# Performance work log

Hardware: AMD Instinct MI355X
Metric: run time of the kernel (lower is better)

## Reference

```python
import jax, jax.numpy as jnp
import numpy as np

B, T, C = 4, 2048, 1024
H, HS = 16, 64  # n_heads, head_size; H*HS == C


def setup_inputs() -> dict:
    key = jax.random.key(0)
    ks = jax.random.split(key, 6)
    s = 0.02
    x = jax.random.normal(ks[0], (B, T, C), dtype=jnp.float32)
    Wq = jax.random.normal(ks[1], (H, C, HS), dtype=jnp.float32) * s
    Wk = jax.random.normal(ks[2], (H, C, HS), dtype=jnp.float32) * s
    Wv = jax.random.normal(ks[3], (H, C, HS), dtype=jnp.float32) * s
    Wo = jax.random.normal(ks[4], (C, C), dtype=jnp.float32) * s
    bo = jnp.zeros((C,), dtype=jnp.float32)
    return {"x": x, "Wq": Wq, "Wk": Wk, "Wv": Wv, "Wo": Wo, "bo": bo}


def reference(x, Wq, Wk, Wv, Wo, bo):
    # batched multi-head causal attention (math identical to per-head loop)
    q = jnp.einsum('btc,hcd->bhtd', x, Wq)  # [B,H,T,HS]
    k = jnp.einsum('btc,hcd->bhtd', x, Wk)
    v = jnp.einsum('btc,hcd->bhtd', x, Wv)
    scale = 1.0 / jnp.sqrt(jnp.asarray(HS, x.dtype))
    scores = jnp.einsum('bhtd,bhsd->bhts', q, k) * scale  # [B,H,T,T]
    causal = jnp.tril(jnp.ones((T, T), dtype=bool))
    scores = jnp.where(causal, scores, jnp.asarray(-jnp.inf, scores.dtype))
    attn = jax.nn.softmax(scores, axis=-1)
    out = jnp.einsum('bhts,bhsd->bhtd', attn, v)  # [B,H,T,HS]
    # concat heads along feature dim (head order == module list order)
    out = out.transpose(0, 2, 1, 3).reshape(B, T, C)
    return out @ Wo.T + bo
```

## Files before the change

### kernel.cpp

```cpp
#include <hip/hip_runtime.h>

typedef __attribute__((ext_vector_type(8))) short v8s;
typedef __attribute__((ext_vector_type(4))) short v4s;
typedef __attribute__((ext_vector_type(4))) float v4f;

static __device__ __forceinline__ short f2bf(float f) {
  union { float f; unsigned u; } c; c.f = f;
  unsigned r = c.u + 0x7fffu + ((c.u >> 16) & 1u);
  return (short)(r >> 16);
}

static __device__ __forceinline__ unsigned pk_bf16(float a, float b) {
  union { float f; unsigned u; } ca, cb; ca.f = a; cb.f = b;
  return ((ca.u + 0x8000u) >> 16) | ((cb.u + 0x8000u) & 0xffff0000u);
}

#if __has_builtin(__builtin_amdgcn_exp2f)
#define EXP2(x) __builtin_amdgcn_exp2f(x)
#else
#define EXP2(x) exp2f(x)
#endif

#define GLDS(gp, lp) __builtin_amdgcn_global_load_lds( \
    (const __attribute__((address_space(1))) void*)(gp), \
    (__attribute__((address_space(3))) void*)(lp), 16, 0, 0)


__global__ __launch_bounds__(256) void cast_f32_bf16(const float* __restrict__ src,
                                                     short* __restrict__ dst) {
  int idx = (blockIdx.x * 256 + threadIdx.x) * 4;
  float4 v = *(const float4*)(src + idx);
  v4s o; o.x = f2bf(v.x); o.y = f2bf(v.y); o.z = f2bf(v.z); o.w = f2bf(v.w);
  *(v4s*)(dst + idx) = o;
}

__global__ __launch_bounds__(256) void build_wt(const float* __restrict__ Wq,
                                                const float* __restrict__ Wk,
                                                const float* __restrict__ Wv,
                                                short* __restrict__ Wt) {
  __shared__ float tile[64][65];
  int blk = blockIdx.x;
  int sel = blk >> 8, rest = blk & 255;
  int h = rest >> 4, kt = rest & 15;
  const float* W = (sel == 0) ? Wq : ((sel == 1) ? Wk : Wv);
  int k0 = kt * 64;
  int tid = threadIdx.x;
  for (int i = 0; i < 4; ++i) {
    int c = i * 256 + tid;
    int row = c >> 4, c4 = (c & 15) * 4;
    float4 v = *(const float4*)(W + (size_t)h * 65536 + (size_t)(k0 + row) * 64 + c4);
    tile[row][c4 + 0] = v.x; tile[row][c4 + 1] = v.y;
    tile[row][c4 + 2] = v.z; tile[row][c4 + 3] = v.w;
  }
  __syncthreads();
  for (int i = 0; i < 2; ++i) {
    int c = i * 256 + tid;
    int d = c >> 3, k8 = (c & 7) * 8;
    v8s o;
    for (int j = 0; j < 8; ++j) o[j] = f2bf(tile[k8 + j][d]);
    *(v8s*)(Wt + (size_t)(sel * 1024 + h * 64 + d) * 1024 + k0 + k8) = o;
  }
}


__global__ __launch_bounds__(512) void gemm_qkv(const short* __restrict__ Xb,
                                                const short* __restrict__ Wt,
                                                short* __restrict__ Qo,
                                                short* __restrict__ Ko,
                                                short* __restrict__ Vt) {
  __shared__ short lds[49152];
  const int tid = threadIdx.x;
  const int lane = tid & 63, quad = lane >> 4, l16 = lane & 15;
  const int wave = tid >> 6;
  const int m0 = blockIdx.x * 256, n0 = blockIdx.y * 128;
  const int wm = (wave >> 1) * 64, wn = (wave & 1) * 64;

  const int r0 = tid >> 2, cbs = (tid & 3) ^ ((r0 >> 1) & 3);
  const size_t offA0 = (size_t)(m0 + r0) * 1024 + cbs * 8;
  const size_t offB0 = (size_t)(n0 + r0) * 1024 + cbs * 8;

  int aoff[4], boff[4];
#pragma unroll
  for (int mt = 0; mt < 4; ++mt) {
    int row = wm + mt * 16 + l16;
    aoff[mt] = row * 32 + (quad ^ ((row >> 1) & 3)) * 8;
  }
#pragma unroll
  for (int nt = 0; nt < 4; ++nt) {
    int row = wn + nt * 16 + l16;
    boff[nt] = row * 32 + (quad ^ ((row >> 1) & 3)) * 8;
  }

  v4f acc[4][4];
#pragma unroll
  for (int i = 0; i < 4; ++i)
#pragma unroll
    for (int j = 0; j < 4; ++j) acc[i][j] = (v4f){0.f, 0.f, 0.f, 0.f};

#pragma unroll
  for (int t = 0; t < 3; ++t) {
    GLDS(Xb + offA0 + t * 32, lds + t * 8192 + tid * 8);
    GLDS(Xb + offA0 + 131072 + t * 32, lds + t * 8192 + 4096 + tid * 8);
    GLDS(Wt + offB0 + t * 32, lds + 32768 + t * 4096 + tid * 8);
  }
  asm volatile("s_waitcnt vmcnt(6)" ::: "memory");
  __builtin_amdgcn_s_barrier();

#pragma unroll 4
  for (int t = 0; t < 32; ++t) {
    const int p = t & 3;
    int tn = t + 3; if (tn > 31) tn = 31;
    const int pn = (t + 3) & 3;
    const short* lAp = lds + p * 8192;
    const short* lBp = lds + 32768 + p * 4096;

    GLDS(Xb + offA0 + tn * 32, lds + pn * 8192 + tid * 8);
    GLDS(Xb + offA0 + 131072 + tn * 32, lds + pn * 8192 + 4096 + tid * 8);
    v8s a[4], b[2];
#pragma unroll
    for (int mt = 0; mt < 4; ++mt) a[mt] = *(const v8s*)(lAp + aoff[mt]);
    b[0] = *(const v8s*)(lBp + boff[0]);
    b[1] = *(const v8s*)(lBp + boff[1]);
    __builtin_amdgcn_s_setprio(1);
#pragma unroll
    for (int mt = 0; mt < 4; ++mt) {
      acc[mt][0] = __builtin_amdgcn_mfma_f32_16x16x32_bf16(a[mt], b[0], acc[mt][0], 0, 0, 0);
      acc[mt][1] = __builtin_amdgcn_mfma_f32_16x16x32_bf16(a[mt], b[1], acc[mt][1], 0, 0, 0);
    }
    __builtin_amdgcn_s_setprio(0);

    GLDS(Wt + offB0 + tn * 32, lds + 32768 + pn * 4096 + tid * 8);
    b[0] = *(const v8s*)(lBp + boff[2]);
    b[1] = *(const v8s*)(lBp + boff[3]);
    __builtin_amdgcn_s_setprio(1);
#pragma unroll
    for (int mt = 0; mt < 4; ++mt) {
      acc[mt][2] = __builtin_amdgcn_mfma_f32_16x16x32_bf16(a[mt], b[0], acc[mt][2], 0, 0, 0);
      acc[mt][3] = __builtin_amdgcn_mfma_f32_16x16x32_bf16(a[mt], b[1], acc[mt][3], 0, 0, 0);
    }
    __builtin_amdgcn_s_setprio(0);

    asm volatile("s_waitcnt vmcnt(6) lgkmcnt(0)" ::: "memory");
    __builtin_amdgcn_s_barrier();
  }

  const int selu = n0 >> 10;
  if (selu < 2) {
    short* obase = (selu == 0) ? Qo : Ko;
#pragma unroll
    for (int nt = 0; nt < 4; ++nt) {
      int n = (n0 + wn + nt * 16 + l16) & 1023;
      int h = n >> 6, d = n & 63;
#pragma unroll
      for (int mt = 0; mt < 4; ++mt) {
        int m = m0 + wm + mt * 16 + quad * 4;
        int b_ = m >> 11, tt = m & 2047;
        size_t base = (size_t)((b_ * 16 + h) * 2048 + tt) * 64 + d;
#pragma unroll
        for (int r = 0; r < 4; ++r)
          obase[base + (size_t)r * 64] = f2bf(acc[mt][nt][r]);
      }
    }
  } else {
#pragma unroll
    for (int nt = 0; nt < 4; ++nt) {
      int n = (n0 + wn + nt * 16 + l16) & 1023;
      int h = n >> 6, d = n & 63;
#pragma unroll
      for (int mt = 0; mt < 4; ++mt) {
        int m = m0 + wm + mt * 16 + quad * 4;
        int b_ = m >> 11, tt = m & 2047;
        int2 dw;
        dw.x = (int)pk_bf16(acc[mt][nt][0], acc[mt][nt][1]);
        dw.y = (int)pk_bf16(acc[mt][nt][2], acc[mt][nt][3]);
        *(int2*)(Vt + ((size_t)(b_ * 16 + h) * 64 + d) * 2048 + tt) = dw;
      }
    }
  }
}


__global__ __launch_bounds__(256, 2) void attn(const short* __restrict__ Q,
                                               const short* __restrict__ K,
                                               const short* __restrict__ Vt,
                                               short* __restrict__ AO) {
  __shared__ short lK[64 * 64];
  __shared__ short lV[64 * 64];
  __shared__ short lP[4 * 32 * 72];
  const int tid = threadIdx.x;
  const int w = tid >> 6, lane = tid & 63, quad = lane >> 4, l16 = lane & 15;
  const int bh = blockIdx.x & 63, pr = blockIdx.x >> 6;
  const float kexp = 0.18033688011112042f;
  const unsigned psel = 0x07060302u;
  short* pw = lP + w * (32 * 72);
  const size_t qkbase = (size_t)bh * 2048 * 64;
  const size_t vtbase = (size_t)bh * 64 * 2048;
  const int b_ = bh >> 4, h = bh & 15;

  const int r0 = tid >> 3, cp = tid & 7;
  const int cl0 = cp ^ (r0 & 7);
  const int r1 = r0 + 32;
  const int cl1 = cp ^ (r1 & 7);

  const int swz = l16 & 7;
  const int ph0 = (quad ^ swz) * 8;
  const int ph1 = ((quad + 4) ^ swz) * 8;

  for (int phase = 0; phase < 2; ++phase) {
    const int c = phase ? (15 - pr) : pr;
    const int qc = c * 128 + w * 32;

    v8s bQ[2][2];
#pragma unroll
    for (int qs = 0; qs < 2; ++qs) {
      const short* qb = Q + qkbase + (size_t)(qc + qs * 16 + l16) * 64 + quad * 8;
      bQ[qs][0] = *(const v8s*)(qb);
      bQ[qs][1] = *(const v8s*)(qb + 32);
    }
    v4f accO[2][4];
#pragma unroll
    for (int qs = 0; qs < 2; ++qs)
      for (int g = 0; g < 4; ++g) accO[qs][g] = (v4f){0.f, 0.f, 0.f, 0.f};
    float lrun[2] = {0.f, 0.f};

    const int nst = 2 * c + 2;
    for (int kt = 0; kt < nst; ++kt) {
      const int kb = kt * 64;
      __syncthreads();
      GLDS(K + qkbase + (size_t)(kb + r0) * 64 + cl0 * 8, lK + tid * 8);
      GLDS(K + qkbase + (size_t)(kb + r1) * 64 + cl1 * 8, lK + tid * 8 + 2048);
      GLDS(Vt + vtbase + (size_t)r0 * 2048 + kb + cl0 * 8, lV + tid * 8);
      GLDS(Vt + vtbase + (size_t)r1 * 2048 + kb + cl1 * 8, lV + tid * 8 + 2048);
      __syncthreads();

      const bool act0 = kb < qc + 16;
      const bool act1 = kb < qc + 32;
      if (!act1) continue;

      v8s aK[4][2];
#pragma unroll
      for (int mt = 0; mt < 4; ++mt) {
        const short* kr = lK + (mt * 16 + l16) * 64;
        aK[mt][0] = *(const v8s*)(kr + ph0);
        aK[mt][1] = *(const v8s*)(kr + ph1);
      }
#pragma unroll
      for (int qs = 0; qs < 2; ++qs) {
        if (qs == 0 ? !act0 : false) continue;
        const int rbase = qc + qs * 16;
        v4f sT[4];
#pragma unroll
        for (int mt = 0; mt < 4; ++mt) {
          v4f t = (v4f){0.f, 0.f, 0.f, 0.f};
          t = __builtin_amdgcn_mfma_f32_16x16x32_bf16(aK[mt][0], bQ[qs][0], t, 0, 0, 0);
          t = __builtin_amdgcn_mfma_f32_16x16x32_bf16(aK[mt][1], bQ[qs][1], t, 0, 0, 0);
          sT[mt] = t;
        }
        if (kb + 63 >= rbase) {
          const int kq = kb + quad * 4 - (rbase + l16);
#pragma unroll
          for (int mt = 0; mt < 4; ++mt)
#pragma unroll
            for (int r = 0; r < 4; ++r)
              if (kq + mt * 16 + r > 0) sT[mt][r] = -__builtin_inff();
        }
        float ls = lrun[qs];
#pragma unroll
        for (int mt = 0; mt < 4; ++mt) {
          float p0 = EXP2(sT[mt][0] * kexp);
          float p1 = EXP2(sT[mt][1] * kexp);
          float p2 = EXP2(sT[mt][2] * kexp);
          float p3 = EXP2(sT[mt][3] * kexp);
          ls += (p0 + p1) + (p2 + p3);
          int2 dw;
          dw.x = (int)__builtin_amdgcn_perm(__float_as_uint(p1), __float_as_uint(p0), psel);
          dw.y = (int)__builtin_amdgcn_perm(__float_as_uint(p3), __float_as_uint(p2), psel);
          *(int2*)&pw[(qs * 16 + l16) * 72 + mt * 16 + quad * 4] = dw;
        }
        lrun[qs] = ls;
      }
      v8s aV[4][2];
#pragma unroll
      for (int g = 0; g < 4; ++g) {
        const short* vr = lV + (g * 16 + l16) * 64;
        aV[g][0] = *(const v8s*)(vr + ph0);
        aV[g][1] = *(const v8s*)(vr + ph1);
      }
#pragma unroll
      for (int qs = 0; qs < 2; ++qs) {
        if (qs == 0 ? !act0 : false) continue;
        v8s bP0 = *(const v8s*)&pw[(qs * 16 + l16) * 72 + quad * 8];
        v8s bP1 = *(const v8s*)&pw[(qs * 16 + l16) * 72 + 32 + quad * 8];
#pragma unroll
        for (int g = 0; g < 4; ++g) {
          accO[qs][g] = __builtin_amdgcn_mfma_f32_16x16x32_bf16(aV[g][0], bP0, accO[qs][g], 0, 0, 0);
          accO[qs][g] = __builtin_amdgcn_mfma_f32_16x16x32_bf16(aV[g][1], bP1, accO[qs][g], 0, 0, 0);
        }
      }
    }

#pragma unroll
    for (int qs = 0; qs < 2; ++qs) {
      float ls = lrun[qs];
      ls += __shfl_xor(ls, 16);
      ls += __shfl_xor(ls, 32);
      float inv = __builtin_amdgcn_rcpf(ls);
      int t = qc + qs * 16 + l16;
      short* ao = AO + ((size_t)(b_ * 2048 + t)) * 1024 + h * 64 + quad * 4;
#pragma unroll
      for (int g = 0; g < 4; ++g) {
        int2 dw;
        dw.x = (int)pk_bf16(accO[qs][g][0] * inv, accO[qs][g][1] * inv);
        dw.y = (int)pk_bf16(accO[qs][g][2] * inv, accO[qs][g][3] * inv);
        *(int2*)(ao + g * 16) = dw;
      }
    }
  }
}


__global__ __launch_bounds__(256) void gemm_out(const short* __restrict__ AO,
                                                const short* __restrict__ Wot,
                                                const float* __restrict__ bo,
                                                float* __restrict__ out) {
  __shared__ short lA[128 * 32];
  __shared__ short lB[128 * 32];
  const int tid = threadIdx.x;
  const int lane = tid & 63, quad = lane >> 4, l16 = lane & 15;
  const int wave = tid >> 6;
  const int m0 = blockIdx.x * 128, n0 = blockIdx.y * 128;
  const int wm = (wave >> 1) * 64, wn = (wave & 1) * 64;
  v4f acc[4][4];
  for (int i = 0; i < 4; ++i)
    for (int j = 0; j < 4; ++j) acc[i][j] = (v4f){0.f, 0.f, 0.f, 0.f};

  for (int k0 = 0; k0 < 1024; k0 += 32) {
    __syncthreads();
    for (int i = 0; i < 2; ++i) {
      int c = i * 256 + tid;
      int row = c >> 2, kc = c & 3;
      GLDS(AO + (size_t)(m0 + row) * 1024 + k0 + kc * 8, lA + c * 8);
      GLDS(Wot + (size_t)(n0 + row) * 1024 + k0 + kc * 8, lB + c * 8);
    }
    __syncthreads();
    v8s a[4], b[4];
    for (int mt = 0; mt < 4; ++mt) a[mt] = *(const v8s*)&lA[(wm + mt * 16 + l16) * 32 + quad * 8];
    for (int nt = 0; nt < 4; ++nt) b[nt] = *(const v8s*)&lB[(wn + nt * 16 + l16) * 32 + quad * 8];
    for (int mt = 0; mt < 4; ++mt)
      for (int nt = 0; nt < 4; ++nt)
        acc[mt][nt] = __builtin_amdgcn_mfma_f32_16x16x32_bf16(a[mt], b[nt], acc[mt][nt], 0, 0, 0);
  }

  for (int nt = 0; nt < 4; ++nt) {
    int n = n0 + wn + nt * 16 + l16;
    float bias = bo[n];
    for (int mt = 0; mt < 4; ++mt)
      for (int r = 0; r < 4; ++r) {
        int m = m0 + wm + mt * 16 + quad * 4 + r;
        out[(size_t)m * 1024 + n] = acc[mt][nt][r] + bias;
      }
  }
}


extern "C" void kernel_launch(void* const* d_in, const int* in_sizes, int n_in,
                              void* d_out, int out_size, void* d_ws, size_t ws_size,
                              hipStream_t stream) {
  const float* x  = (const float*)d_in[0];
  const float* Wq = (const float*)d_in[1];
  const float* Wk = (const float*)d_in[2];
  const float* Wv = (const float*)d_in[3];
  const float* Wo = (const float*)d_in[4];
  const float* bo = (const float*)d_in[5];
  float* out = (float*)d_out;
  char* ws = (char*)d_ws;

  short* Xb  = (short*)(ws);
  short* Wt  = (short*)(ws + (16u << 20));
  short* Wot = (short*)(ws + (22u << 20));
  short* Q   = (short*)(ws + (24u << 20));
  short* K   = (short*)(ws + (40u << 20));
  short* Vt  = (short*)(ws + (56u << 20));

  cast_f32_bf16<<<8192, 256, 0, stream>>>(x, Xb);
  cast_f32_bf16<<<1024, 256, 0, stream>>>(Wo, Wot);
  build_wt<<<768, 256, 0, stream>>>(Wq, Wk, Wv, Wt);
  gemm_qkv<<<dim3(32, 24), 512, 0, stream>>>(Xb, Wt, Q, K, Vt);
  attn<<<dim3(512), 256, 0, stream>>>(Q, K, Vt, Xb);
  gemm_out<<<dim3(64, 8), 256, 0, stream>>>(Xb, Wot, bo, out);
}
```

Baseline: 243.0 us.

## Restructure QKV GEMM pipeline with XCD-aware tiling and enlarge attention query tiles

The QKV GEMM moves to a K-step of 64, a double-buffered LDS schedule with interleaved barriers and set-priority phases, and a block-index remap that groups tiles per XCD for L2 locality. The attention kernel drops the two-phase paired-chunk loop: each block now handles one 256-row query chunk, with each wave covering 64 rows, and chunks are mapped so blocks with complementary causal work are paired. The aim is fewer global K/V reloads per query row and more MFMA work per barrier. The cost is higher register pressure (accO grows to 4x4) and possible load imbalance across blocks.

```diff
diff --git a/kernel.cpp b/kernel.cpp
--- a/kernel.cpp
+++ b/kernel.cpp
@@ -63,6 +63,55 @@
 }
 
 
+#define GQ_STAGE_A(P, T) do {                                                     \
+  _Pragma("unroll") for (int i_ = 0; i_ < 4; ++i_)                                \
+    GLDS(Xb + (size_t)(m0 + rA + i_ * 64) * 1024 + (T) * 64 + cbl * 8,            \
+         lds + (P) * 16384 + (tid + i_ * 512) * 8); } while (0)
+
+#define GQ_STAGE_B(P, T) do {                                                     \
+  _Pragma("unroll") for (int i_ = 0; i_ < 2; ++i_)                                \
+    GLDS(Wt + (size_t)(n0 + rA + i_ * 64) * 1024 + (T) * 64 + cbl * 8,            \
+         lds + 32768 + (P) * 8192 + (tid + i_ * 512) * 8); } while (0)
+
+#define PH_MID()                                                                  \
+  __builtin_amdgcn_s_barrier();                                                   \
+  asm volatile("s_waitcnt lgkmcnt(0)" ::: "memory");                              \
+  __builtin_amdgcn_sched_barrier(0);                                              \
+  __builtin_amdgcn_s_setprio(1)
+
+#define PH_END()                                                                  \
+  __builtin_amdgcn_s_setprio(0);                                                  \
+  __builtin_amdgcn_s_barrier()
+
+#define LD_A(P, KS) _Pragma("unroll") for (int mt = 0; mt < 4; ++mt)              \
+    a[mt] = *(const v8s*)(lds + (P) * 16384 + arow[mt] + ((KS) ? csw1 : csw0));
+
+#define LD_B2(P, N0, KS)                                                          \
+  bb[0] = *(const v8s*)(lds + 32768 + (P) * 8192 + brow[N0] + ((KS) ? csw1 : csw0)); \
+  bb[1] = *(const v8s*)(lds + 32768 + (P) * 8192 + brow[(N0) + 1] + ((KS) ? csw1 : csw0));
+
+#define MF2(N0) _Pragma("unroll") for (int mt = 0; mt < 4; ++mt) {                \
+    acc[mt][N0] = __builtin_amdgcn_mfma_f32_16x16x32_bf16(a[mt], bb[0], acc[mt][N0], 0, 0, 0); \
+    acc[mt][(N0) + 1] = __builtin_amdgcn_mfma_f32_16x16x32_bf16(a[mt], bb[1], acc[mt][(N0) + 1], 0, 0, 0); }
+
+#define KTILE(P, T) {                                                             \
+  const int q_ = (P) ^ 1;                                                         \
+  const int tn1 = ((T) + 1 < 16) ? (T) + 1 : 15;                                  \
+  const int tn2 = ((T) + 2 < 16) ? (T) + 2 : 15;                                  \
+  LD_A(P, 0); LD_B2(P, 0, 0);                                                     \
+  GQ_STAGE_B(q_, tn1);                                                            \
+  PH_MID(); MF2(0); PH_END();                                                     \
+  LD_B2(P, 2, 0);                                                                 \
+  PH_MID(); MF2(2); PH_END();                                                     \
+  LD_A(P, 1); LD_B2(P, 0, 1);                                                     \
+  PH_MID(); MF2(0); PH_END();                                                     \
+  LD_B2(P, 2, 1);                                                                 \
+  GQ_STAGE_A(P, tn2);                                                             \
+  PH_MID(); MF2(2);                                                               \
+  __builtin_amdgcn_s_setprio(0);                                                  \
+  asm volatile("s_waitcnt vmcnt(4)" ::: "memory");                                \
+  __builtin_amdgcn_s_barrier(); }
+
 __global__ __launch_bounds__(512) void gemm_qkv(const short* __restrict__ Xb,
                                                 const short* __restrict__ Wt,
                                                 short* __restrict__ Qo,
@@ -72,77 +121,42 @@
   const int tid = threadIdx.x;
   const int lane = tid & 63, quad = lane >> 4, l16 = lane & 15;
   const int wave = tid >> 6;
-  const int m0 = blockIdx.x * 256, n0 = blockIdx.y * 128;
+  const int bid = blockIdx.x;
+  const int xcd = bid & 7, rr = bid >> 3;
+  const int m0 = ((xcd >> 1) * 8 + (rr & 7)) * 256;
+  const int n0 = ((xcd & 1) * 12 + (rr >> 3)) * 128;
   const int wm = (wave >> 1) * 64, wn = (wave & 1) * 64;
 
-  const int r0 = tid >> 2, cbs = (tid & 3) ^ ((r0 >> 1) & 3);
-  const size_t offA0 = (size_t)(m0 + r0) * 1024 + cbs * 8;
-  const size_t offB0 = (size_t)(n0 + r0) * 1024 + cbs * 8;
-
-  int aoff[4], boff[4];
-#pragma unroll
-  for (int mt = 0; mt < 4; ++mt) {
-    int row = wm + mt * 16 + l16;
-    aoff[mt] = row * 32 + (quad ^ ((row >> 1) & 3)) * 8;
-  }
-#pragma unroll
-  for (int nt = 0; nt < 4; ++nt) {
-    int row = wn + nt * 16 + l16;
-    boff[nt] = row * 32 + (quad ^ ((row >> 1) & 3)) * 8;
-  }
+  const int rA = tid >> 3;
+  const int cbl = (tid & 7) ^ (rA & 7);
+
+  const int swz = l16 & 7;
+  const int csw0 = (quad ^ swz) * 8;
+  const int csw1 = ((4 + quad) ^ swz) * 8;
+  int arow[4], brow[4];
+#pragma unroll
+  for (int mt = 0; mt < 4; ++mt) arow[mt] = (wm + mt * 16 + l16) * 64;
+#pragma unroll
+  for (int nt = 0; nt < 4; ++nt) brow[nt] = (wn + nt * 16 + l16) * 64;
 
   v4f acc[4][4];
 #pragma unroll
   for (int i = 0; i < 4; ++i)
 #pragma unroll
     for (int j = 0; j < 4; ++j) acc[i][j] = (v4f){0.f, 0.f, 0.f, 0.f};
-
-#pragma unroll
-  for (int t = 0; t < 3; ++t) {
-    GLDS(Xb + offA0 + t * 32, lds + t * 8192 + tid * 8);
-    GLDS(Xb + offA0 + 131072 + t * 32, lds + t * 8192 + 4096 + tid * 8);
-    GLDS(Wt + offB0 + t * 32, lds + 32768 + t * 4096 + tid * 8);
-  }
-  asm volatile("s_waitcnt vmcnt(6)" ::: "memory");
+  v8s a[4], bb[2];
+
+  GQ_STAGE_A(0, 0); GQ_STAGE_B(0, 0); GQ_STAGE_A(1, 1);
+  asm volatile("s_waitcnt vmcnt(4)" ::: "memory");
   __builtin_amdgcn_s_barrier();
 
-#pragma unroll 4
-  for (int t = 0; t < 32; ++t) {
-    const int p = t & 3;
-    int tn = t + 3; if (tn > 31) tn = 31;
-    const int pn = (t + 3) & 3;
-    const short* lAp = lds + p * 8192;
-    const short* lBp = lds + 32768 + p * 4096;
-
-    GLDS(Xb + offA0 + tn * 32, lds + pn * 8192 + tid * 8);
-    GLDS(Xb + offA0 + 131072 + tn * 32, lds + pn * 8192 + 4096 + tid * 8);
-    v8s a[4], b[2];
-#pragma unroll
-    for (int mt = 0; mt < 4; ++mt) a[mt] = *(const v8s*)(lAp + aoff[mt]);
-    b[0] = *(const v8s*)(lBp + boff[0]);
-    b[1] = *(const v8s*)(lBp + boff[1]);
-    __builtin_amdgcn_s_setprio(1);
-#pragma unroll
-    for (int mt = 0; mt < 4; ++mt) {
-      acc[mt][0] = __builtin_amdgcn_mfma_f32_16x16x32_bf16(a[mt], b[0], acc[mt][0], 0, 0, 0);
-      acc[mt][1] = __builtin_amdgcn_mfma_f32_16x16x32_bf16(a[mt], b[1], acc[mt][1], 0, 0, 0);
-    }
-    __builtin_amdgcn_s_setprio(0);
-
-    GLDS(Wt + offB0 + tn * 32, lds + 32768 + pn * 4096 + tid * 8);
-    b[0] = *(const v8s*)(lBp + boff[2]);
-    b[1] = *(const v8s*)(lBp + boff[3]);
-    __builtin_amdgcn_s_setprio(1);
-#pragma unroll
-    for (int mt = 0; mt < 4; ++mt) {
-      acc[mt][2] = __builtin_amdgcn_mfma_f32_16x16x32_bf16(a[mt], b[0], acc[mt][2], 0, 0, 0);
-      acc[mt][3] = __builtin_amdgcn_mfma_f32_16x16x32_bf16(a[mt], b[1], acc[mt][3], 0, 0, 0);
-    }
-    __builtin_amdgcn_s_setprio(0);
-
-    asm volatile("s_waitcnt vmcnt(6) lgkmcnt(0)" ::: "memory");
-    __builtin_amdgcn_s_barrier();
-  }
+#pragma unroll 1
+  for (int tt = 0; tt < 8; ++tt) {
+    const int t0 = tt * 2;
+    KTILE(0, t0);
+    KTILE(1, t0 + 1);
+  }
+  asm volatile("s_waitcnt vmcnt(0)" ::: "memory");
 
   const int selu = n0 >> 10;
   if (selu < 2) {
@@ -154,8 +168,8 @@
 #pragma unroll
       for (int mt = 0; mt < 4; ++mt) {
         int m = m0 + wm + mt * 16 + quad * 4;
-        int b_ = m >> 11, tt = m & 2047;
-        size_t base = (size_t)((b_ * 16 + h) * 2048 + tt) * 64 + d;
+        int b_ = m >> 11, tt_ = m & 2047;
+        size_t base = (size_t)((b_ * 16 + h) * 2048 + tt_) * 64 + d;
 #pragma unroll
         for (int r = 0; r < 4; ++r)
           obase[base + (size_t)r * 64] = f2bf(acc[mt][nt][r]);
@@ -169,15 +183,24 @@
 #pragma unroll
       for (int mt = 0; mt < 4; ++mt) {
         int m = m0 + wm + mt * 16 + quad * 4;
-        int b_ = m >> 11, tt = m & 2047;
+        int b_ = m >> 11, tt_ = m & 2047;
         int2 dw;
         dw.x = (int)pk_bf16(acc[mt][nt][0], acc[mt][nt][1]);
         dw.y = (int)pk_bf16(acc[mt][nt][2], acc[mt][nt][3]);
-        *(int2*)(Vt + ((size_t)(b_ * 16 + h) * 64 + d) * 2048 + tt) = dw;
-      }
-    }
-  }
-}
+        *(int2*)(Vt + ((size_t)(b_ * 16 + h) * 64 + d) * 2048 + tt_) = dw;
+      }
+    }
+  }
+}
+
+#undef KTILE
+#undef LD_A
+#undef LD_B2
+#undef MF2
+#undef PH_MID
+#undef PH_END
+#undef GQ_STAGE_A
+#undef GQ_STAGE_B
 
 
 __global__ __launch_bounds__(256, 2) void attn(const short* __restrict__ Q,
@@ -186,13 +209,15 @@
                                                short* __restrict__ AO) {
   __shared__ short lK[64 * 64];
   __shared__ short lV[64 * 64];
-  __shared__ short lP[4 * 32 * 72];
+  __shared__ short lP[4 * 64 * 72];
   const int tid = threadIdx.x;
   const int w = tid >> 6, lane = tid & 63, quad = lane >> 4, l16 = lane & 15;
-  const int bh = blockIdx.x & 63, pr = blockIdx.x >> 6;
+  const int bh = blockIdx.x & 63;
+  const int u = blockIdx.x >> 6;
+  const int c = (u < 4) ? u : 11 - u;
   const float kexp = 0.18033688011112042f;
   const unsigned psel = 0x07060302u;
-  short* pw = lP + w * (32 * 72);
+  short* pw = lP + w * (64 * 72);
   const size_t qkbase = (size_t)bh * 2048 * 64;
   const size_t vtbase = (size_t)bh * 64 * 2048;
   const int b_ = bh >> 4, h = bh & 15;
@@ -206,114 +231,114 @@
   const int ph0 = (quad ^ swz) * 8;
   const int ph1 = ((quad + 4) ^ swz) * 8;
 
-  for (int phase = 0; phase < 2; ++phase) {
-    const int c = phase ? (15 - pr) : pr;
-    const int qc = c * 128 + w * 32;
-
-    v8s bQ[2][2];
-#pragma unroll
-    for (int qs = 0; qs < 2; ++qs) {
-      const short* qb = Q + qkbase + (size_t)(qc + qs * 16 + l16) * 64 + quad * 8;
-      bQ[qs][0] = *(const v8s*)(qb);
-      bQ[qs][1] = *(const v8s*)(qb + 32);
-    }
-    v4f accO[2][4];
-#pragma unroll
-    for (int qs = 0; qs < 2; ++qs)
-      for (int g = 0; g < 4; ++g) accO[qs][g] = (v4f){0.f, 0.f, 0.f, 0.f};
-    float lrun[2] = {0.f, 0.f};
-
-    const int nst = 2 * c + 2;
-    for (int kt = 0; kt < nst; ++kt) {
-      const int kb = kt * 64;
-      __syncthreads();
-      GLDS(K + qkbase + (size_t)(kb + r0) * 64 + cl0 * 8, lK + tid * 8);
-      GLDS(K + qkbase + (size_t)(kb + r1) * 64 + cl1 * 8, lK + tid * 8 + 2048);
-      GLDS(Vt + vtbase + (size_t)r0 * 2048 + kb + cl0 * 8, lV + tid * 8);
-      GLDS(Vt + vtbase + (size_t)r1 * 2048 + kb + cl1 * 8, lV + tid * 8 + 2048);
-      __syncthreads();
-
-      const bool act0 = kb < qc + 16;
-      const bool act1 = kb < qc + 32;
-      if (!act1) continue;
-
-      v8s aK[4][2];
+  const int qc = c * 256 + w * 64;
+
+  v8s bQ[4][2];
+#pragma unroll
+  for (int qs = 0; qs < 4; ++qs) {
+    const short* qb = Q + qkbase + (size_t)(qc + qs * 16 + l16) * 64 + quad * 8;
+    bQ[qs][0] = *(const v8s*)(qb);
+    bQ[qs][1] = *(const v8s*)(qb + 32);
+  }
+  v4f accO[4][4];
+#pragma unroll
+  for (int qs = 0; qs < 4; ++qs)
+#pragma unroll
+    for (int g = 0; g < 4; ++g) accO[qs][g] = (v4f){0.f, 0.f, 0.f, 0.f};
+  float lrun[4] = {0.f, 0.f, 0.f, 0.f};
+
+  const int nst = 4 * c + 4;
+  for (int kt = 0; kt < nst; ++kt) {
+    const int kb = kt * 64;
+    __syncthreads();
+    GLDS(K + qkbase + (size_t)(kb + r0) * 64 + cl0 * 8, lK + tid * 8);
+    GLDS(K + qkbase + (size_t)(kb + r1) * 64 + cl1 * 8, lK + tid * 8 + 2048);
+    GLDS(Vt + vtbase + (size_t)r0 * 2048 + kb + cl0 * 8, lV + tid * 8);
+    GLDS(Vt + vtbase + (size_t)r1 * 2048 + kb + cl1 * 8, lV + tid * 8 + 2048);
+    __syncthreads();
+
+    if (kb >= qc + 64) continue;
+
+    v8s aK[4][2];
+#pragma unroll
+    for (int mt = 0; mt < 4; ++mt) {
+      const short* kr = lK + (mt * 16 + l16) * 64;
+      aK[mt][0] = *(const v8s*)(kr + ph0);
+      aK[mt][1] = *(const v8s*)(kr + ph1);
+    }
+#pragma unroll
+    for (int qs = 0; qs < 4; ++qs) {
+      const int rbase = qc + qs * 16;
+      if (kb >= rbase + 16) continue;
+      v4f sT[4];
+      __builtin_amdgcn_s_setprio(1);
 #pragma unroll
       for (int mt = 0; mt < 4; ++mt) {
-        const short* kr = lK + (mt * 16 + l16) * 64;
-        aK[mt][0] = *(const v8s*)(kr + ph0);
-        aK[mt][1] = *(const v8s*)(kr + ph1);
-      }
-#pragma unroll
-      for (int qs = 0; qs < 2; ++qs) {
-        if (qs == 0 ? !act0 : false) continue;
-        const int rbase = qc + qs * 16;
-        v4f sT[4];
-#pragma unroll
-        for (int mt = 0; mt < 4; ++mt) {
-          v4f t = (v4f){0.f, 0.f, 0.f, 0.f};
-          t = __builtin_amdgcn_mfma_f32_16x16x32_bf16(aK[mt][0], bQ[qs][0], t, 0, 0, 0);
-          t = __builtin_amdgcn_mfma_f32_16x16x32_bf16(aK[mt][1], bQ[qs][1], t, 0, 0, 0);
-          sT[mt] = t;
-        }
-        if (kb + 63 >= rbase) {
-          const int kq = kb + quad * 4 - (rbase + l16);
-#pragma unroll
-          for (int mt = 0; mt < 4; ++mt)
-#pragma unroll
-            for (int r = 0; r < 4; ++r)
-              if (kq + mt * 16 + r > 0) sT[mt][r] = -__builtin_inff();
-        }
-        float ls = lrun[qs];
-#pragma unroll
-        for (int mt = 0; mt < 4; ++mt) {
-          float p0 = EXP2(sT[mt][0] * kexp);
-          float p1 = EXP2(sT[mt][1] * kexp);
-          float p2 = EXP2(sT[mt][2] * kexp);
-          float p3 = EXP2(sT[mt][3] * kexp);
-          ls += (p0 + p1) + (p2 + p3);
-          int2 dw;
-          dw.x = (int)__builtin_amdgcn_perm(__float_as_uint(p1), __float_as_uint(p0), psel);
-          dw.y = (int)__builtin_amdgcn_perm(__float_as_uint(p3), __float_as_uint(p2), psel);
-          *(int2*)&pw[(qs * 16 + l16) * 72 + mt * 16 + quad * 4] = dw;
-        }
-        lrun[qs] = ls;
-      }
-      v8s aV[4][2];
+        v4f t = (v4f){0.f, 0.f, 0.f, 0.f};
+        t = __builtin_amdgcn_mfma_f32_16x16x32_bf16(aK[mt][0], bQ[qs][0], t, 0, 0, 0);
+        t = __builtin_amdgcn_mfma_f32_16x16x32_bf16(aK[mt][1], bQ[qs][1], t, 0, 0, 0);
+        sT[mt] = t;
+      }
+      __builtin_amdgcn_s_setprio(0);
+      if (kb + 63 >= rbase) {
+        const int kq = kb + quad * 4 - (rbase + l16);
+#pragma unroll
+        for (int mt = 0; mt < 4; ++mt)
+#pragma unroll
+          for (int r = 0; r < 4; ++r)
+            if (kq + mt * 16 + r > 0) sT[mt][r] = -__builtin_inff();
+      }
+      float ls = lrun[qs];
+#pragma unroll
+      for (int mt = 0; mt < 4; ++mt) {
+        float p0 = EXP2(sT[mt][0] * kexp);
+        float p1 = EXP2(sT[mt][1] * kexp);
+        float p2 = EXP2(sT[mt][2] * kexp);
+        float p3 = EXP2(sT[mt][3] * kexp);
+        ls += (p0 + p1) + (p2 + p3);
+        int2 dw;
+        dw.x = (int)__builtin_amdgcn_perm(__float_as_uint(p1), __float_as_uint(p0), psel);
+        dw.y = (int)__builtin_amdgcn_perm(__float_as_uint(p3), __float_as_uint(p2), psel);
+        *(int2*)&pw[(qs * 16 + l16) * 72 + mt * 16 + quad * 4] = dw;
+      }
+      lrun[qs] = ls;
+    }
+    v8s aV[4][2];
+#pragma unroll
+    for (int g = 0; g < 4; ++g) {
+      const short* vr = lV + (g * 16 + l16) * 64;
+      aV[g][0] = *(const v8s*)(vr + ph0);
+      aV[g][1] = *(const v8s*)(vr + ph1);
+    }
+#pragma unroll
+    for (int qs = 0; qs < 4; ++qs) {
+      if (kb >= qc + qs * 16 + 16) continue;
+      v8s bP0 = *(const v8s*)&pw[(qs * 16 + l16) * 72 + quad * 8];
+      v8s bP1 = *(const v8s*)&pw[(qs * 16 + l16) * 72 + 32 + quad * 8];
+      __builtin_amdgcn_s_setprio(1);
 #pragma unroll
       for (int g = 0; g < 4; ++g) {
-        const short* vr = lV + (g * 16 + l16) * 64;
-        aV[g][0] = *(const v8s*)(vr + ph0);
-        aV[g][1] = *(const v8s*)(vr + ph1);
-      }
-#pragma unroll
-      for (int qs = 0; qs < 2; ++qs) {
-        if (qs == 0 ? !act0 : false) continue;
-        v8s bP0 = *(const v8s*)&pw[(qs * 16 + l16) * 72 + quad * 8];
-        v8s bP1 = *(const v8s*)&pw[(qs * 16 + l16) * 72 + 32 + quad * 8];
-#pragma unroll
-        for (int g = 0; g < 4; ++g) {
-          accO[qs][g] = __builtin_amdgcn_mfma_f32_16x16x32_bf16(aV[g][0], bP0, accO[qs][g], 0, 0, 0);
-          accO[qs][g] = __builtin_amdgcn_mfma_f32_16x16x32_bf16(aV[g][1], bP1, accO[qs][g], 0, 0, 0);
-        }
-      }
-    }
-
-#pragma unroll
-    for (int qs = 0; qs < 2; ++qs) {
-      float ls = lrun[qs];
-      ls += __shfl_xor(ls, 16);
-      ls += __shfl_xor(ls, 32);
-      float inv = __builtin_amdgcn_rcpf(ls);
-      int t = qc + qs * 16 + l16;
-      short* ao = AO + ((size_t)(b_ * 2048 + t)) * 1024 + h * 64 + quad * 4;
-#pragma unroll
-      for (int g = 0; g < 4; ++g) {
-        int2 dw;
-        dw.x = (int)pk_bf16(accO[qs][g][0] * inv, accO[qs][g][1] * inv);
-        dw.y = (int)pk_bf16(accO[qs][g][2] * inv, accO[qs][g][3] * inv);
-        *(int2*)(ao + g * 16) = dw;
-      }
+        accO[qs][g] = __builtin_amdgcn_mfma_f32_16x16x32_bf16(aV[g][0], bP0, accO[qs][g], 0, 0, 0);
+        accO[qs][g] = __builtin_amdgcn_mfma_f32_16x16x32_bf16(aV[g][1], bP1, accO[qs][g], 0, 0, 0);
+      }
+      __builtin_amdgcn_s_setprio(0);
+    }
+  }
+
+#pragma unroll
+  for (int qs = 0; qs < 4; ++qs) {
+    float ls = lrun[qs];
+    ls += __shfl_xor(ls, 16);
+    ls += __shfl_xor(ls, 32);
+    float inv = __builtin_amdgcn_rcpf(ls);
+    int t = qc + qs * 16 + l16;
+    short* ao = AO + ((size_t)(b_ * 2048 + t)) * 1024 + h * 64 + quad * 4;
+#pragma unroll
+    for (int g = 0; g < 4; ++g) {
+      int2 dw;
+      dw.x = (int)pk_bf16(accO[qs][g][0] * inv, accO[qs][g][1] * inv);
+      dw.y = (int)pk_bf16(accO[qs][g][2] * inv, accO[qs][g][3] * inv);
+      *(int2*)(ao + g * 16) = dw;
     }
   }
 }
@@ -385,7 +410,7 @@
   cast_f32_bf16<<<8192, 256, 0, stream>>>(x, Xb);
   cast_f32_bf16<<<1024, 256, 0, stream>>>(Wo, Wot);
   build_wt<<<768, 256, 0, stream>>>(Wq, Wk, Wv, Wt);
-  gemm_qkv<<<dim3(32, 24), 512, 0, stream>>>(Xb, Wt, Q, K, Vt);
+  gemm_qkv<<<768, 512, 0, stream>>>(Xb, Wt, Q, K, Vt);
   attn<<<dim3(512), 256, 0, stream>>>(Q, K, Vt, Xb);
   gemm_out<<<dim3(64, 8), 256, 0, stream>>>(Xb, Wot, bo, out);
 }
```

Result: slower. 262.3 us (+7.9%).

## Fuse prep kernels, double-buffer attention K/V loads, pipeline output GEMM

Applied to the files above, without the earlier changes.

Three separate changes. The three preprocessing launches (x cast, Wo cast, QKV weight transpose) become a single prep kernel, which removes launch overhead. The attention kernel now double-buffers K/V tiles in LDS, prefetching the next tile before computing the current one, and raises wave priority around the MFMA blocks. The output GEMM moves to 512 threads, 256x128 tiles, a 4-stage LDS prefetch pipeline and swizzled LDS addressing. The extra LDS use in attention may reduce occupancy, and the partial waitcnt logic has to be exact to stay correct.

```diff
diff --git a/kernel.cpp b/kernel.cpp
--- a/kernel.cpp
+++ b/kernel.cpp
@@ -26,25 +26,32 @@
     (__attribute__((address_space(3))) void*)(lp), 16, 0, 0)
 
 
-__global__ __launch_bounds__(256) void cast_f32_bf16(const float* __restrict__ src,
-                                                     short* __restrict__ dst) {
-  int idx = (blockIdx.x * 256 + threadIdx.x) * 4;
-  float4 v = *(const float4*)(src + idx);
-  v4s o; o.x = f2bf(v.x); o.y = f2bf(v.y); o.z = f2bf(v.z); o.w = f2bf(v.w);
-  *(v4s*)(dst + idx) = o;
-}
-
-__global__ __launch_bounds__(256) void build_wt(const float* __restrict__ Wq,
-                                                const float* __restrict__ Wk,
-                                                const float* __restrict__ Wv,
-                                                short* __restrict__ Wt) {
+__global__ __launch_bounds__(256) void prep(const float* __restrict__ x,
+                                            const float* __restrict__ Wq,
+                                            const float* __restrict__ Wk,
+                                            const float* __restrict__ Wv,
+                                            const float* __restrict__ Wo,
+                                            short* __restrict__ Xb,
+                                            short* __restrict__ Wot,
+                                            short* __restrict__ Wt) {
   __shared__ float tile[64][65];
-  int blk = blockIdx.x;
-  int sel = blk >> 8, rest = blk & 255;
-  int h = rest >> 4, kt = rest & 15;
+  const int blk = blockIdx.x;
+  const int tid = threadIdx.x;
+  if (blk < 9216) {
+    const float* src = (blk < 8192) ? x : Wo;
+    short* dst = (blk < 8192) ? Xb : Wot;
+    const int b2 = (blk < 8192) ? blk : (blk - 8192);
+    const int idx = (b2 * 256 + tid) * 4;
+    float4 v = *(const float4*)(src + idx);
+    v4s o; o.x = f2bf(v.x); o.y = f2bf(v.y); o.z = f2bf(v.z); o.w = f2bf(v.w);
+    *(v4s*)(dst + idx) = o;
+    return;
+  }
+  const int bb = blk - 9216;
+  const int sel = bb >> 8, rest = bb & 255;
+  const int h = rest >> 4, kt = rest & 15;
   const float* W = (sel == 0) ? Wq : ((sel == 1) ? Wk : Wv);
-  int k0 = kt * 64;
-  int tid = threadIdx.x;
+  const int k0 = kt * 64;
   for (int i = 0; i < 4; ++i) {
     int c = i * 256 + tid;
     int row = c >> 4, c4 = (c & 15) * 4;
@@ -154,8 +161,8 @@
 #pragma unroll
       for (int mt = 0; mt < 4; ++mt) {
         int m = m0 + wm + mt * 16 + quad * 4;
-        int b_ = m >> 11, tt = m & 2047;
-        size_t base = (size_t)((b_ * 16 + h) * 2048 + tt) * 64 + d;
+        int b_ = m >> 11, tt_ = m & 2047;
+        size_t base = (size_t)((b_ * 16 + h) * 2048 + tt_) * 64 + d;
 #pragma unroll
         for (int r = 0; r < 4; ++r)
           obase[base + (size_t)r * 64] = f2bf(acc[mt][nt][r]);
@@ -169,23 +176,29 @@
 #pragma unroll
       for (int mt = 0; mt < 4; ++mt) {
         int m = m0 + wm + mt * 16 + quad * 4;
-        int b_ = m >> 11, tt = m & 2047;
+        int b_ = m >> 11, tt_ = m & 2047;
         int2 dw;
         dw.x = (int)pk_bf16(acc[mt][nt][0], acc[mt][nt][1]);
         dw.y = (int)pk_bf16(acc[mt][nt][2], acc[mt][nt][3]);
-        *(int2*)(Vt + ((size_t)(b_ * 16 + h) * 64 + d) * 2048 + tt) = dw;
+        *(int2*)(Vt + ((size_t)(b_ * 16 + h) * 64 + d) * 2048 + tt_) = dw;
       }
     }
   }
 }
 
+
+#define ASTAGE(P, KB)                                                             \
+  GLDS(K + qkbase + (size_t)((KB) + r0) * 64 + cl0 * 8, lK + (P) * 4096 + tid * 8);          \
+  GLDS(K + qkbase + (size_t)((KB) + r1) * 64 + cl1 * 8, lK + (P) * 4096 + tid * 8 + 2048);   \
+  GLDS(Vt + vtbase + (size_t)r0 * 2048 + (KB) + cl0 * 8, lV + (P) * 4096 + tid * 8);         \
+  GLDS(Vt + vtbase + (size_t)r1 * 2048 + (KB) + cl1 * 8, lV + (P) * 4096 + tid * 8 + 2048)
 
 __global__ __launch_bounds__(256, 2) void attn(const short* __restrict__ Q,
                                                const short* __restrict__ K,
                                                const short* __restrict__ Vt,
                                                short* __restrict__ AO) {
-  __shared__ short lK[64 * 64];
-  __shared__ short lV[64 * 64];
+  __shared__ short lK[2 * 64 * 64];
+  __shared__ short lV[2 * 64 * 64];
   __shared__ short lP[4 * 32 * 72];
   const int tid = threadIdx.x;
   const int w = tid >> 6, lane = tid & 63, quad = lane >> 4, l16 = lane & 15;
@@ -224,79 +237,92 @@
     float lrun[2] = {0.f, 0.f};
 
     const int nst = 2 * c + 2;
+
+    __builtin_amdgcn_s_barrier();
+    ASTAGE(0, 0);
+
     for (int kt = 0; kt < nst; ++kt) {
+      const int p = kt & 1;
       const int kb = kt * 64;
-      __syncthreads();
-      GLDS(K + qkbase + (size_t)(kb + r0) * 64 + cl0 * 8, lK + tid * 8);
-      GLDS(K + qkbase + (size_t)(kb + r1) * 64 + cl1 * 8, lK + tid * 8 + 2048);
-      GLDS(Vt + vtbase + (size_t)r0 * 2048 + kb + cl0 * 8, lV + tid * 8);
-      GLDS(Vt + vtbase + (size_t)r1 * 2048 + kb + cl1 * 8, lV + tid * 8 + 2048);
-      __syncthreads();
+      if (kt + 1 < nst) {
+        ASTAGE(p ^ 1, kb + 64);
+        asm volatile("s_waitcnt vmcnt(4)" ::: "memory");
+      } else {
+        asm volatile("s_waitcnt vmcnt(0)" ::: "memory");
+      }
+      __builtin_amdgcn_s_barrier();
+      const short* lKp = lK + p * 4096;
+      const short* lVp = lV + p * 4096;
 
       const bool act0 = kb < qc + 16;
       const bool act1 = kb < qc + 32;
-      if (!act1) continue;
-
-      v8s aK[4][2];
-#pragma unroll
-      for (int mt = 0; mt < 4; ++mt) {
-        const short* kr = lK + (mt * 16 + l16) * 64;
-        aK[mt][0] = *(const v8s*)(kr + ph0);
-        aK[mt][1] = *(const v8s*)(kr + ph1);
-      }
-#pragma unroll
-      for (int qs = 0; qs < 2; ++qs) {
-        if (qs == 0 ? !act0 : false) continue;
-        const int rbase = qc + qs * 16;
-        v4f sT[4];
+      if (act1) {
+        v8s aK[4][2];
 #pragma unroll
         for (int mt = 0; mt < 4; ++mt) {
-          v4f t = (v4f){0.f, 0.f, 0.f, 0.f};
-          t = __builtin_amdgcn_mfma_f32_16x16x32_bf16(aK[mt][0], bQ[qs][0], t, 0, 0, 0);
-          t = __builtin_amdgcn_mfma_f32_16x16x32_bf16(aK[mt][1], bQ[qs][1], t, 0, 0, 0);
-          sT[mt] = t;
+          const short* kr = lKp + (mt * 16 + l16) * 64;
+          aK[mt][0] = *(const v8s*)(kr + ph0);
+          aK[mt][1] = *(const v8s*)(kr + ph1);
         }
-        if (kb + 63 >= rbase) {
-          const int kq = kb + quad * 4 - (rbase + l16);
-#pragma unroll
-          for (int mt = 0; mt < 4; ++mt)
-#pragma unroll
-            for (int r = 0; r < 4; ++r)
-              if (kq + mt * 16 + r > 0) sT[mt][r] = -__builtin_inff();
+#pragma unroll
+        for (int qs = 0; qs < 2; ++qs) {
+          if (qs == 0 ? !act0 : false) continue;
+          const int rbase = qc + qs * 16;
+          v4f sT[4];
+          __builtin_amdgcn_s_setprio(1);
+#pragma unroll
+          for (int mt = 0; mt < 4; ++mt) {
+            v4f t = (v4f){0.f, 0.f, 0.f, 0.f};
+            t = __builtin_amdgcn_mfma_f32_16x16x32_bf16(aK[mt][0], bQ[qs][0], t, 0, 0, 0);
+            t = __builtin_amdgcn_mfma_f32_16x16x32_bf16(aK[mt][1], bQ[qs][1], t, 0, 0, 0);
+            sT[mt] = t;
+          }
+          __builtin_amdgcn_s_setprio(0);
+          if (kb + 63 >= rbase) {
+            const int kq = kb + quad * 4 - (rbase + l16);
+#pragma unroll
+            for (int mt = 0; mt < 4; ++mt)
+#pragma unroll
+              for (int r = 0; r < 4; ++r)
+                if (kq + mt * 16 + r > 0) sT[mt][r] = -__builtin_inff();
+          }
+          float ls = lrun[qs];
+#pragma unroll
+          for (int mt = 0; mt < 4; ++mt) {
+            float p0 = EXP2(sT[mt][0] * kexp);
+            float p1 = EXP2(sT[mt][1] * kexp);
+            float p2 = EXP2(sT[mt][2] * kexp);
+            float p3 = EXP2(sT[mt][3] * kexp);
+            ls += (p0 + p1) + (p2 + p3);
+            int2 dw;
+            dw.x = (int)__builtin_amdgcn_perm(__float_as_uint(p1), __float_as_uint(p0), psel);
+            dw.y = (int)__builtin_amdgcn_perm(__float_as_uint(p3), __float_as_uint(p2), psel);
+            *(int2*)&pw[(qs * 16 + l16) * 72 + mt * 16 + quad * 4] = dw;
+          }
+          lrun[qs] = ls;
         }
-        float ls = lrun[qs];
-#pragma unroll
-        for (int mt = 0; mt < 4; ++mt) {
-          float p0 = EXP2(sT[mt][0] * kexp);
-          float p1 = EXP2(sT[mt][1] * kexp);
-          float p2 = EXP2(sT[mt][2] * kexp);
-          float p3 = EXP2(sT[mt][3] * kexp);
-          ls += (p0 + p1) + (p2 + p3);
-          int2 dw;
-          dw.x = (int)__builtin_amdgcn_perm(__float_as_uint(p1), __float_as_uint(p0), psel);
-          dw.y = (int)__builtin_amdgcn_perm(__float_as_uint(p3), __float_as_uint(p2), psel);
-          *(int2*)&pw[(qs * 16 + l16) * 72 + mt * 16 + quad * 4] = dw;
+        v8s aV[4][2];
+#pragma unroll
+        for (int g = 0; g < 4; ++g) {
+          const short* vr = lVp + (g * 16 + l16) * 64;
+          aV[g][0] = *(const v8s*)(vr + ph0);
+          aV[g][1] = *(const v8s*)(vr + ph1);
         }
-        lrun[qs] = ls;
-      }
-      v8s aV[4][2];
-#pragma unroll
-      for (int g = 0; g < 4; ++g) {
-        const short* vr = lV + (g * 16 + l16) * 64;
-        aV[g][0] = *(const v8s*)(vr + ph0);
-        aV[g][1] = *(const v8s*)(vr + ph1);
-      }
-#pragma unroll
-      for (int qs = 0; qs < 2; ++qs) {
-        if (qs == 0 ? !act0 : false) continue;
-        v8s bP0 = *(const v8s*)&pw[(qs * 16 + l16) * 72 + quad * 8];
-        v8s bP1 = *(const v8s*)&pw[(qs * 16 + l16) * 72 + 32 + quad * 8];
-#pragma unroll
-        for (int g = 0; g < 4; ++g) {
-          accO[qs][g] = __builtin_amdgcn_mfma_f32_16x16x32_bf16(aV[g][0], bP0, accO[qs][g], 0, 0, 0);
-          accO[qs][g] = __builtin_amdgcn_mfma_f32_16x16x32_bf16(aV[g][1], bP1, accO[qs][g], 0, 0, 0);
+#pragma unroll
+        for (int qs = 0; qs < 2; ++qs) {
+          if (qs == 0 ? !act0 : false) continue;
+          v8s bP0 = *(const v8s*)&pw[(qs * 16 + l16) * 72 + quad * 8];
+          v8s bP1 = *(const v8s*)&pw[(qs * 16 + l16) * 72 + 32 + quad * 8];
+          __builtin_amdgcn_s_setprio(1);
+#pragma unroll
+          for (int g = 0; g < 4; ++g) {
+            accO[qs][g] = __builtin_amdgcn_mfma_f32_16x16x32_bf16(aV[g][0], bP0, accO[qs][g], 0, 0, 0);
+            accO[qs][g] = __builtin_amdgcn_mfma_f32_16x16x32_bf16(aV[g][1], bP1, accO[qs][g], 0, 0, 0);
+          }
+          __builtin_amdgcn_s_setprio(0);
         }
       }
+      __builtin_amdgcn_s_barrier();
     }
 
 #pragma unroll
@@ -318,47 +344,100 @@
   }
 }
 
-
-__global__ __launch_bounds__(256) void gemm_out(const short* __restrict__ AO,
+#undef ASTAGE
+
+
+__global__ __launch_bounds__(512) void gemm_out(const short* __restrict__ AO,
                                                 const short* __restrict__ Wot,
                                                 const float* __restrict__ bo,
                                                 float* __restrict__ out) {
-  __shared__ short lA[128 * 32];
-  __shared__ short lB[128 * 32];
+  __shared__ short lds[49152];
   const int tid = threadIdx.x;
   const int lane = tid & 63, quad = lane >> 4, l16 = lane & 15;
   const int wave = tid >> 6;
-  const int m0 = blockIdx.x * 128, n0 = blockIdx.y * 128;
+  const int m0 = blockIdx.x * 256, n0 = blockIdx.y * 128;
   const int wm = (wave >> 1) * 64, wn = (wave & 1) * 64;
+
+  const int r0 = tid >> 2, cbs = (tid & 3) ^ ((r0 >> 1) & 3);
+  const size_t offA0 = (size_t)(m0 + r0) * 1024 + cbs * 8;
+  const size_t offB0 = (size_t)(n0 + r0) * 1024 + cbs * 8;
+
+  int aoff[4], boff[4];
+#pragma unroll
+  for (int mt = 0; mt < 4; ++mt) {
+    int row = wm + mt * 16 + l16;
+    aoff[mt] = row * 32 + (quad ^ ((row >> 1) & 3)) * 8;
+  }
+#pragma unroll
+  for (int nt = 0; nt < 4; ++nt) {
+    int row = wn + nt * 16 + l16;
+    boff[nt] = row * 32 + (quad ^ ((row >> 1) & 3)) * 8;
+  }
+
   v4f acc[4][4];
+#pragma unroll
   for (int i = 0; i < 4; ++i)
+#pragma unroll
     for (int j = 0; j < 4; ++j) acc[i][j] = (v4f){0.f, 0.f, 0.f, 0.f};
 
-  for (int k0 = 0; k0 < 1024; k0 += 32) {
-    __syncthreads();
-    for (int i = 0; i < 2; ++i) {
-      int c = i * 256 + tid;
-      int row = c >> 2, kc = c & 3;
-      GLDS(AO + (size_t)(m0 + row) * 1024 + k0 + kc * 8, lA + c * 8);
-      GLDS(Wot + (size_t)(n0 + row) * 1024 + k0 + kc * 8, lB + c * 8);
-    }
-    __syncthreads();
-    v8s a[4], b[4];
-    for (int mt = 0; mt < 4; ++mt) a[mt] = *(const v8s*)&lA[(wm + mt * 16 + l16) * 32 + quad * 8];
-    for (int nt = 0; nt < 4; ++nt) b[nt] = *(const v8s*)&lB[(wn + nt * 16 + l16) * 32 + quad * 8];
-    for (int mt = 0; mt < 4; ++mt)
-      for (int nt = 0; nt < 4; ++nt)
-        acc[mt][nt] = __builtin_amdgcn_mfma_f32_16x16x32_bf16(a[mt], b[nt], acc[mt][nt], 0, 0, 0);
-  }
-
+#pragma unroll
+  for (int t = 0; t < 3; ++t) {
+    GLDS(AO + offA0 + t * 32, lds + t * 8192 + tid * 8);
+    GLDS(AO + offA0 + 131072 + t * 32, lds + t * 8192 + 4096 + tid * 8);
+    GLDS(Wot + offB0 + t * 32, lds + 32768 + t * 4096 + tid * 8);
+  }
+  asm volatile("s_waitcnt vmcnt(6)" ::: "memory");
+  __builtin_amdgcn_s_barrier();
+
+#pragma unroll 4
+  for (int t = 0; t < 32; ++t) {
+    const int p = t & 3;
+    int tn = t + 3; if (tn > 31) tn = 31;
+    const int pn = (t + 3) & 3;
+    const short* lAp = lds + p * 8192;
+    const short* lBp = lds + 32768 + p * 4096;
+
+    GLDS(AO + offA0 + tn * 32, lds + pn * 8192 + tid * 8);
+    GLDS(AO + offA0 + 131072 + tn * 32, lds + pn * 8192 + 4096 + tid * 8);
+    v8s a[4], b[2];
+#pragma unroll
+    for (int mt = 0; mt < 4; ++mt) a[mt] = *(const v8s*)(lAp + aoff[mt]);
+    b[0] = *(const v8s*)(lBp + boff[0]);
+    b[1] = *(const v8s*)(lBp + boff[1]);
+    __builtin_amdgcn_s_setprio(1);
+#pragma unroll
+    for (int mt = 0; mt < 4; ++mt) {
+      acc[mt][0] = __builtin_amdgcn_mfma_f32_16x16x32_bf16(a[mt], b[0], acc[mt][0], 0, 0, 0);
+      acc[mt][1] = __builtin_amdgcn_mfma_f32_16x16x32_bf16(a[mt], b[1], acc[mt][1], 0, 0, 0);
+    }
+    __builtin_amdgcn_s_setprio(0);
+
+    GLDS(Wot + offB0 + tn * 32, lds + 32768 + pn * 4096 + tid * 8);
+    b[0] = *(const v8s*)(lBp + boff[2]);
+    b[1] = *(const v8s*)(lBp + boff[3]);
+    __builtin_amdgcn_s_setprio(1);
+#pragma unroll
+    for (int mt = 0; mt < 4; ++mt) {
+      acc[mt][2] = __builtin_amdgcn_mfma_f32_16x16x32_bf16(a[mt], b[0], acc[mt][2], 0, 0, 0);
+      acc[mt][3] = __builtin_amdgcn_mfma_f32_16x16x32_bf16(a[mt], b[1], acc[mt][3], 0, 0, 0);
+    }
+    __builtin_amdgcn_s_setprio(0);
+
+    asm volatile("s_waitcnt vmcnt(6) lgkmcnt(0)" ::: "memory");
+    __builtin_amdgcn_s_barrier();
+  }
+
+#pragma unroll
   for (int nt = 0; nt < 4; ++nt) {
     int n = n0 + wn + nt * 16 + l16;
     float bias = bo[n];
-    for (int mt = 0; mt < 4; ++mt)
-      for (int r = 0; r < 4; ++r) {
-        int m = m0 + wm + mt * 16 + quad * 4 + r;
-        out[(size_t)m * 1024 + n] = acc[mt][nt][r] + bias;
-      }
+#pragma unroll
+    for (int mt = 0; mt < 4; ++mt) {
+      int m = m0 + wm + mt * 16 + quad * 4;
+#pragma unroll
+      for (int r = 0; r < 4; ++r)
+        out[(size_t)(m + r) * 1024 + n] = acc[mt][nt][r] + bias;
+    }
   }
 }
 
@@ -382,10 +461,8 @@
   short* K   = (short*)(ws + (40u << 20));
   short* Vt  = (short*)(ws + (56u << 20));
 
-  cast_f32_bf16<<<8192, 256, 0, stream>>>(x, Xb);
-  cast_f32_bf16<<<1024, 256, 0, stream>>>(Wo, Wot);
-  build_wt<<<768, 256, 0, stream>>>(Wq, Wk, Wv, Wt);
+  prep<<<9984, 256, 0, stream>>>(x, Wq, Wk, Wv, Wo, Xb, Wot, Wt);
   gemm_qkv<<<dim3(32, 24), 512, 0, stream>>>(Xb, Wt, Q, K, Vt);
   attn<<<dim3(512), 256, 0, stream>>>(Q, K, Vt, Xb);
-  gemm_out<<<dim3(64, 8), 256, 0, stream>>>(Xb, Wot, bo, out);
-}
+  gemm_out<<<dim3(32, 8), 512, 0, stream>>>(Xb, Wot, bo, out);
+}
```

Measured after the change: 231.3 us. -4.8%, faster.
